# Kernel optimization log

Hardware: AMD Instinct MI355X
Metric: run time of the kernel (lower is better)

The kernel has to match this reference:

```python
import jax, jax.numpy as jnp
from jax import lax
import numpy as np

B, H, W, C = 32, 56, 56, 384
NH, WS, SS = 12, 7, 3
HD = C // NH
N = WS * WS
HID = 384  # int(mlp_ratio*dim / reduce_scale) = int(4*384/4)
SCALE = HD ** -0.5
L = H * W


def _rel_pos_index():
    coords = np.stack(np.meshgrid(np.arange(WS), np.arange(WS), indexing='ij'))
    cf = coords.reshape(2, -1)
    rc = (cf[:, :, None] - cf[:, None, :]).transpose(1, 2, 0)
    rc[..., 0] += WS - 1
    rc[..., 1] += WS - 1
    rc[..., 0] *= 2 * WS - 1
    return rc.sum(-1).reshape(-1)  # (N*N,)


def _win_part_np(x):
    b, h, w, c = x.shape
    x = x.reshape(b, h // WS, WS, w // WS, WS, c).transpose(0, 1, 3, 2, 4, 5)
    return x.reshape(-1, WS, WS, c)


def _attn_mask():
    img = np.zeros((1, H, W, 1), np.float32)
    cnt = 0
    sl = (slice(0, -WS), slice(-WS, -SS), slice(-SS, None))
    for hs in sl:
        for ws in sl:
            img[:, hs, ws, :] = cnt
            cnt += 1
    mw = _win_part_np(img).reshape(-1, N)
    am = mw[:, None, :] - mw[:, :, None]
    return np.where(am != 0, -100.0, 0.0).astype(np.float32)  # (nW, N, N)


REL_IDX = _rel_pos_index()
ATTN_MASK = _attn_mask()


def window_partition(x):  # (B,H,W,C) -> (B*nW, N, C)
    x = x.reshape(B, H // WS, WS, W // WS, WS, C).transpose(0, 1, 3, 2, 4, 5)
    return x.reshape(-1, N, C)


def window_reverse(wins):  # (B*nW, N, C) -> (B,H,W,C)
    x = wins.reshape(B, H // WS, W // WS, WS, WS, C).transpose(0, 1, 3, 2, 4, 5)
    return x.reshape(B, H, W, C)


def _ln(x, g, b):
    m = x.mean(-1, keepdims=True)
    v = ((x - m) ** 2).mean(-1, keepdims=True)
    return (x - m) * lax.rsqrt(v + 1e-5) * g + b


def setup_inputs() -> dict:
    key = jax.random.key(0)
    ks = iter(jax.random.split(key, 16))
    w = lambda shape: jax.random.normal(next(ks), shape, jnp.float32) * 0.02
    return {
        'x': jax.random.normal(next(ks), (B, L, C), jnp.float32),
        'norm1_g': jnp.ones((C,), jnp.float32), 'norm1_b': jnp.zeros((C,), jnp.float32),
        'qkv_w': w((3 * C, C)), 'qkv_b': jnp.zeros((3 * C,), jnp.float32),
        'rpb_table': w(((2 * WS - 1) ** 2, NH)),
        'proj_w': w((C, C)), 'proj_b': jnp.zeros((C,), jnp.float32),
        'se1_w': w((C // 2, C)), 'se1_b': jnp.zeros((C // 2,), jnp.float32),
        'se2_w': w((C, C // 2)), 'se2_b': jnp.zeros((C,), jnp.float32),
        'norm2_g': jnp.ones((C,), jnp.float32), 'norm2_b': jnp.zeros((C,), jnp.float32),
        'c1_w': w((HID, C)), 'c1_b': jnp.zeros((HID,), jnp.float32),
        'bn1_g': jnp.ones((HID,), jnp.float32), 'bn1_b': jnp.zeros((HID,), jnp.float32),
        'dw_w': w((HID, 1, 3, 3)), 'dw_b': jnp.zeros((HID,), jnp.float32),
        'bn2_g': jnp.ones((HID,), jnp.float32), 'bn2_b': jnp.zeros((HID,), jnp.float32),
        'c2_w': w((C, HID)), 'c2_b': jnp.zeros((C,), jnp.float32),
        'bn3_g': jnp.ones((C,), jnp.float32), 'bn3_b': jnp.zeros((C,), jnp.float32),
    }


def reference(x, norm1_g, norm1_b, qkv_w, qkv_b, rpb_table, proj_w, proj_b,
              se1_w, se1_b, se2_w, se2_b, norm2_g, norm2_b,
              c1_w, c1_b, bn1_g, bn1_b, dw_w, dw_b, bn2_g, bn2_b,
              c2_w, c2_b, bn3_g, bn3_b):
    shortcut = x
    h = _ln(x, norm1_g, norm1_b).reshape(B, H, W, C)
    h = jnp.roll(h, (-SS, -SS), axis=(1, 2))           # cyclic shift (SW-MSA)
    win = window_partition(h)                            # (B*nW, N, C)
    qkv = (win @ qkv_w.T + qkv_b).reshape(-1, N, 3, NH, HD).transpose(2, 0, 3, 1, 4)
    q, k, v = qkv[0] * SCALE, qkv[1], qkv[2]             # (B*nW, NH, N, HD)
    attn = jnp.einsum('bhnd,bhmd->bhnm', q, k)           # (B*nW, NH, N, N)
    rpb = rpb_table[jnp.asarray(REL_IDX)].reshape(N, N, NH).transpose(2, 0, 1)
    attn = attn + rpb[None]
    mask = jnp.asarray(ATTN_MASK)                        # (nW, N, N)
    nW = mask.shape[0]
    attn = (attn.reshape(B, nW, NH, N, N) + mask[None, :, None]).reshape(-1, NH, N, N)
    attn = jax.nn.softmax(attn, axis=-1)
    out = jnp.einsum('bhnm,bhmd->bhnd', attn, v).transpose(0, 2, 1, 3).reshape(-1, N, C)
    out = out @ proj_w.T + proj_b
    h = window_reverse(out)
    h = jnp.roll(h, (SS, SS), axis=(1, 2)).reshape(B, L, C)
    x = shortcut + h
    # SE gating, applied token-wise over channel dim exactly as ChannelSELayer_SA
    g = jax.nn.relu(x @ se1_w.T + se1_b)
    g = jax.nn.sigmoid(g @ se2_w.T + se2_b)
    x = x * g
    # light conv MLP branch (Mlp_Light); BatchNorm in eval mode with running
    # mean 0 / var 1 -> pure per-channel affine
    y = _ln(x, norm2_g, norm2_b).reshape(B, H, W, C).transpose(0, 3, 1, 2)  # NCHW
    y = jnp.einsum('bchw,oc->bohw', y, c1_w) + c1_b[None, :, None, None]     # 1x1 conv
    y = jax.nn.gelu(y, approximate=False) * bn1_g[None, :, None, None] + bn1_b[None, :, None, None]
    y = lax.conv_general_dilated(y, dw_w, (1, 1), 'SAME', feature_group_count=HID,
                                 dimension_numbers=('NCHW', 'OIHW', 'NCHW')) + dw_b[None, :, None, None]
    y = jax.nn.gelu(y, approximate=False) * bn2_g[None, :, None, None] + bn2_b[None, :, None, None]
    y = jnp.einsum('bchw,oc->bohw', y, c2_w) + c2_b[None, :, None, None]     # 1x1 conv
    y = y * bn3_g[None, :, None, None] + bn3_b[None, :, None, None]
    x = x + y.transpose(0, 2, 3, 1).reshape(B, L, C)
    return x
```

## Files before the change

kernel.cpp:

```cpp
#include <hip/hip_runtime.h>
#include <hip/hip_bf16.h>

typedef __attribute__((ext_vector_type(4))) float f32x4;
typedef __attribute__((ext_vector_type(8))) __bf16 bf16x8;
typedef __attribute__((ext_vector_type(8))) unsigned short u16x8;

#define SCALE_ 0.17677669529663687f
#define RS 19267584

#define OFF_R1 77070336ull
#define OFF_WB 154140672ull
#define OFF_WT 156205056ull
#define OFF_SB 156218880ull

__device__ __forceinline__ __bf16 tobf(float f) {
  __hip_bfloat16 h = __float2bfloat16(f);
  return __builtin_bit_cast(__bf16, h);
}
__device__ __forceinline__ unsigned short f2u(float f) {
  return __builtin_bit_cast(unsigned short, __float2bfloat16(f));
}

__global__ __launch_bounds__(256) void cvt_kernel(const float* __restrict__ src,
                                                  __hip_bfloat16* __restrict__ dst, int n) {
  int i = blockIdx.x * 256 + threadIdx.x;
  int stride = gridDim.x * 256;
  for (; i < n; i += stride) dst[i] = __float2bfloat16(src[i]);
}

__global__ __launch_bounds__(256) void dwrep_kernel(const float* __restrict__ src,
                                                    float* __restrict__ dst) {
  int i = blockIdx.x * 256 + threadIdx.x;
  if (i < 3456) {
    int c = i / 9, k = i - c * 9;
    dst[k * 384 + c] = src[i];
  }
}

__global__ __launch_bounds__(256) void c1prep_kernel(const float* __restrict__ c1w,
                                                     const float* __restrict__ c1b,
                                                     const float* __restrict__ g,
                                                     const float* __restrict__ b,
                                                     __hip_bfloat16* __restrict__ gc1,
                                                     float* __restrict__ S1,
                                                     float* __restrict__ bb) {
  const int n = blockIdx.x * 4 + (threadIdx.x >> 6);
  const int lane = threadIdx.x & 63;
  float s1 = 0.f, sb = 0.f;
  for (int k = lane; k < 384; k += 64) {
    float w = c1w[n * 384 + k];
    __hip_bfloat16 gw = __float2bfloat16(w * g[k]);
    gc1[n * 384 + k] = gw;
    s1 += __bfloat162float(gw);
    sb += w * b[k];
  }
#pragma unroll
  for (int m = 1; m < 64; m <<= 1) { s1 += __shfl_xor(s1, m, 64); sb += __shfl_xor(sb, m, 64); }
  if (lane == 0) { S1[n] = s1; bb[n] = c1b[n] + sb; }
}

template <bool WIN>
__global__ __launch_bounds__(256) void ln_kernel(const float* __restrict__ x,
                                                 const float* __restrict__ gm,
                                                 const float* __restrict__ bt,
                                                 __hip_bfloat16* __restrict__ out) {
  const int tok = blockIdx.x * 4 + (threadIdx.x >> 6);
  const int lane = threadIdx.x & 63;
  const float2* row = (const float2*)(x + (size_t)tok * 384);
  float2 v[3];
  v[0] = row[lane]; v[1] = row[lane + 64]; v[2] = row[lane + 128];
  float s = 0.f, sq = 0.f;
#pragma unroll
  for (int i = 0; i < 3; ++i) { s += v[i].x + v[i].y; sq += v[i].x * v[i].x + v[i].y * v[i].y; }
#pragma unroll
  for (int m = 1; m < 64; m <<= 1) { s += __shfl_xor(s, m, 64); sq += __shfl_xor(sq, m, 64); }
  const float mean = s * (1.f / 384.f);
  const float var = sq * (1.f / 384.f) - mean * mean;
  const float rstd = rsqrtf(var + 1e-5f);
  size_t dst;
  if constexpr (WIN) {
    int b = tok / 3136, l = tok - b * 3136;
    int i = l / 56, j = l - i * 56;
    int hp = i - 3; if (hp < 0) hp += 56;
    int wp = j - 3; if (wp < 0) wp += 56;
    int wi = (hp / 7) * 8 + wp / 7;
    int n = (hp % 7) * 7 + wp % 7;
    dst = (size_t)(b * 64 + wi) * 49 + n;
  } else {
    dst = (size_t)tok;
  }
  unsigned int* o = (unsigned int*)(out + dst * 384);
  const float2* G = (const float2*)gm;
  const float2* Bv = (const float2*)bt;
#pragma unroll
  for (int i = 0; i < 3; ++i) {
    int j = lane + 64 * i;
    float2 gv = G[j], bv = Bv[j];
    float a = (v[i].x - mean) * rstd * gv.x + bv.x;
    float b2 = (v[i].y - mean) * rstd * gv.y + bv.y;
    o[j] = (unsigned)f2u(a) | ((unsigned)f2u(b2) << 16);
  }
}

enum { EPI_SE2 = 2, EPI_C2 = 4, EPI_QKV = 5 };

template <int EPI, int KD>
__global__ __launch_bounds__(256) void gemm5(const __hip_bfloat16* __restrict__ Ap,
                                             const __hip_bfloat16* __restrict__ W,
                                             const float* __restrict__ bias,
                                             const float* __restrict__ p0,
                                             const float* __restrict__ p1,
                                             const float* __restrict__ p2,
                                             void* __restrict__ outp) {
  constexpr int KS = KD / 32;
  const int tid = threadIdx.x;
  const int lane = tid & 63, wave = tid >> 6;
  const int g = lane >> 4, r = lane & 15;
  const int row0 = blockIdx.x * 64;
  const int col0 = blockIdx.y * 192;
  const int n0 = wave * 48;

  __shared__ __align__(16) __hip_bfloat16 Al[64][40];
  __shared__ __align__(16) __hip_bfloat16 Bl[192][40];

  const int s_row = tid >> 2, s_c = (tid & 3) * 8;
  const size_t arow = (size_t)(row0 + s_row);

  f32x4 acc[4][3] = {};
  bf16x8 a_reg = *(const bf16x8*)(Ap + arow * KD + s_c);
  bf16x8 b_reg[3];
#pragma unroll
  for (int h = 0; h < 3; ++h)
    b_reg[h] = *(const bf16x8*)(W + (size_t)(col0 + s_row + 64 * h) * KD + s_c);

  for (int kk = 0; kk < KS; ++kk) {
    *(bf16x8*)(&Al[s_row][s_c]) = a_reg;
#pragma unroll
    for (int h = 0; h < 3; ++h) *(bf16x8*)(&Bl[s_row + 64 * h][s_c]) = b_reg[h];
    __syncthreads();
    if (kk + 1 < KS) {
      const int kb = (kk + 1) * 32 + s_c;
      a_reg = *(const bf16x8*)(Ap + arow * KD + kb);
#pragma unroll
      for (int h = 0; h < 3; ++h)
        b_reg[h] = *(const bf16x8*)(W + (size_t)(col0 + s_row + 64 * h) * KD + kb);
    }
    bf16x8 af[4];
#pragma unroll
    for (int mt = 0; mt < 4; ++mt) af[mt] = *(const bf16x8*)(&Al[mt * 16 + r][g * 8]);
#pragma unroll
    for (int nt = 0; nt < 3; ++nt) {
      bf16x8 bf = *(const bf16x8*)(&Bl[n0 + nt * 16 + r][g * 8]);
#pragma unroll
      for (int mt = 0; mt < 4; ++mt)
        acc[mt][nt] = __builtin_amdgcn_mfma_f32_16x16x32_bf16(af[mt], bf, acc[mt][nt], 0, 0, 0);
    }
    __syncthreads();
  }

#pragma unroll
  for (int mt = 0; mt < 4; ++mt) {
#pragma unroll
    for (int j = 0; j < 4; ++j) {
      const int row = row0 + mt * 16 + g * 4 + j;
#pragma unroll
      for (int nt = 0; nt < 3; ++nt) {
        const int col = col0 + n0 + nt * 16 + r;
        float v = acc[mt][nt][j] + bias[col];
        if constexpr (EPI == EPI_QKV) {
          const int s = col / 384, cs = col - s * 384;
          if (s == 0) v *= SCALE_;
          ((__hip_bfloat16*)outp)[(size_t)s * RS + (size_t)row * 384 + cs] = __float2bfloat16(v);
        } else if constexpr (EPI == EPI_SE2) {
          float gate = 1.f / (1.f + __expf(-v));
          ((float*)outp)[(size_t)row * 384 + col] = p0[(size_t)row * 384 + col] * gate;
        } else {
          float y = v * p0[col] + p1[col];
          ((float*)outp)[(size_t)row * 384 + col] = p2[(size_t)row * 384 + col] + y;
        }
      }
    }
  }
}

__global__ __launch_bounds__(256) void c1ln_kernel(const float* __restrict__ x2,
                                                   const __hip_bfloat16* __restrict__ gc1,
                                                   const float* __restrict__ S1,
                                                   const float* __restrict__ bb,
                                                   const float* __restrict__ bn1g_,
                                                   const float* __restrict__ bn1b_,
                                                   __hip_bfloat16* __restrict__ y1) {
  const int tid = threadIdx.x;
  const int lane = tid & 63, wave = tid >> 6;
  const int g = lane >> 4, r = lane & 15;
  const int row0 = blockIdx.x * 64;
  const int col0 = blockIdx.y * 192;
  const int n0 = wave * 48;

  __shared__ __align__(16) __hip_bfloat16 Al[64][40];
  __shared__ __align__(16) __hip_bfloat16 Bl[192][40];
  __shared__ float mean_l[64], rstd_l[64];

  const int s_row = tid >> 2, s_c = (tid & 3) * 8;
  const size_t abase = (size_t)(row0 + s_row) * 384;

  {
    float s = 0.f, sq = 0.f;
#pragma unroll
    for (int c = 0; c < 12; ++c) {
      const float4* p = (const float4*)(x2 + abase + c * 32 + s_c);
      float4 a = p[0], b = p[1];
      s += a.x + a.y + a.z + a.w + b.x + b.y + b.z + b.w;
      sq += a.x * a.x + a.y * a.y + a.z * a.z + a.w * a.w +
            b.x * b.x + b.y * b.y + b.z * b.z + b.w * b.w;
    }
#pragma unroll
    for (int m = 1; m < 4; m <<= 1) { s += __shfl_xor(s, m, 64); sq += __shfl_xor(sq, m, 64); }
    if ((tid & 3) == 0) {
      float mean = s * (1.f / 384.f);
      float var = sq * (1.f / 384.f) - mean * mean;
      mean_l[s_row] = mean;
      rstd_l[s_row] = rsqrtf(var + 1e-5f);
    }
  }
  __syncthreads();

  f32x4 acc[4][3] = {};
  bf16x8 a_reg;
  {
    const float4* sp = (const float4*)(x2 + abase + s_c);
    float4 a = sp[0], b = sp[1];
    a_reg[0] = tobf(a.x); a_reg[1] = tobf(a.y); a_reg[2] = tobf(a.z); a_reg[3] = tobf(a.w);
    a_reg[4] = tobf(b.x); a_reg[5] = tobf(b.y); a_reg[6] = tobf(b.z); a_reg[7] = tobf(b.w);
  }
  bf16x8 b_reg[3];
#pragma unroll
  for (int h = 0; h < 3; ++h)
    b_reg[h] = *(const bf16x8*)(gc1 + (size_t)(col0 + s_row + 64 * h) * 384 + s_c);

  for (int kk = 0; kk < 12; ++kk) {
    *(bf16x8*)(&Al[s_row][s_c]) = a_reg;
#pragma unroll
    for (int h = 0; h < 3; ++h) *(bf16x8*)(&Bl[s_row + 64 * h][s_c]) = b_reg[h];
    __syncthreads();
    if (kk + 1 < 12) {
      const int kb = (kk + 1) * 32 + s_c;
      const float4* sp = (const float4*)(x2 + abase + kb);
      float4 a = sp[0], b = sp[1];
      a_reg[0] = tobf(a.x); a_reg[1] = tobf(a.y); a_reg[2] = tobf(a.z); a_reg[3] = tobf(a.w);
      a_reg[4] = tobf(b.x); a_reg[5] = tobf(b.y); a_reg[6] = tobf(b.z); a_reg[7] = tobf(b.w);
#pragma unroll
      for (int h = 0; h < 3; ++h)
        b_reg[h] = *(const bf16x8*)(gc1 + (size_t)(col0 + s_row + 64 * h) * 384 + kb);
    }
    bf16x8 af[4];
#pragma unroll
    for (int mt = 0; mt < 4; ++mt) af[mt] = *(const bf16x8*)(&Al[mt * 16 + r][g * 8]);
#pragma unroll
    for (int nt = 0; nt < 3; ++nt) {
      bf16x8 bf = *(const bf16x8*)(&Bl[n0 + nt * 16 + r][g * 8]);
#pragma unroll
      for (int mt = 0; mt < 4; ++mt)
        acc[mt][nt] = __builtin_amdgcn_mfma_f32_16x16x32_bf16(af[mt], bf, acc[mt][nt], 0, 0, 0);
    }
    __syncthreads();
  }

#pragma unroll
  for (int mt = 0; mt < 4; ++mt) {
#pragma unroll
    for (int j = 0; j < 4; ++j) {
      const int rl = mt * 16 + g * 4 + j;
      const int row = row0 + rl;
      const float mean = mean_l[rl], rstd = rstd_l[rl];
#pragma unroll
      for (int nt = 0; nt < 3; ++nt) {
        const int col = col0 + n0 + nt * 16 + r;
        float v = rstd * (acc[mt][nt][j] - mean * S1[col]) + bb[col];
        float gl = 0.5f * v * (1.f + erff(v * 0.70710678118654752f));
        y1[(size_t)row * 384 + col] = __float2bfloat16(gl * bn1g_[col] + bn1b_[col]);
      }
    }
  }
}

__global__ __launch_bounds__(256) void gemm3_proj(const __hip_bfloat16* __restrict__ Ap,
                                                  const __hip_bfloat16* __restrict__ W,
                                                  const float* __restrict__ bias,
                                                  const float* __restrict__ p0,
                                                  void* __restrict__ outp,
                                                  const __hip_bfloat16* __restrict__ W2,
                                                  const float* __restrict__ bias2,
                                                  void* __restrict__ out2) {
  constexpr int NT = 6;
  const int tid = threadIdx.x;
  const int lane = tid & 63, wave = tid >> 6;
  const int g = lane >> 4, r = lane & 15;
  const int row0 = blockIdx.x * 64;
  const int n0 = wave * 96;

  __shared__ __align__(16) char smem[50176];
  auto Al = (__hip_bfloat16(*)[40])smem;
  auto Bl = (__hip_bfloat16(*)[40])(smem + 64 * 80);

  const int s_row = tid >> 2;
  const int s_c = (tid & 3) * 8;

  size_t arow;
  {
    int t = row0 + s_row;
    int b = t / 3136, l = t - b * 3136;
    int i = l / 56, j = l - i * 56;
    int hp = i >= 3 ? i - 3 : i + 53;
    int wp = j >= 3 ? j - 3 : j + 53;
    arow = ((size_t)(b * 64 + (hp / 7) * 8 + wp / 7)) * 49 + (hp % 7) * 7 + (wp % 7);
  }

  f32x4 acc[4][NT] = {};

  bf16x8 a_reg = *(const bf16x8*)(Ap + arow * 384 + s_c);
  bf16x8 b_reg[NT];
#pragma unroll
  for (int h = 0; h < NT; ++h)
    b_reg[h] = *(const bf16x8*)(W + (size_t)(s_row + 64 * h) * 384 + s_c);

  for (int kk = 0; kk < 12; ++kk) {
    *(bf16x8*)(&Al[s_row][s_c]) = a_reg;
#pragma unroll
    for (int h = 0; h < NT; ++h) *(bf16x8*)(&Bl[s_row + 64 * h][s_c]) = b_reg[h];
    __syncthreads();
    if (kk + 1 < 12) {
      const int kb = (kk + 1) * 32 + s_c;
      a_reg = *(const bf16x8*)(Ap + arow * 384 + kb);
#pragma unroll
      for (int h = 0; h < NT; ++h)
        b_reg[h] = *(const bf16x8*)(W + (size_t)(s_row + 64 * h) * 384 + kb);
    }
    bf16x8 af[4];
#pragma unroll
    for (int mt = 0; mt < 4; ++mt) af[mt] = *(const bf16x8*)(&Al[mt * 16 + r][g * 8]);
#pragma unroll
    for (int nt = 0; nt < NT; ++nt) {
      bf16x8 bf = *(const bf16x8*)(&Bl[n0 + nt * 16 + r][g * 8]);
#pragma unroll
      for (int mt = 0; mt < 4; ++mt)
        acc[mt][nt] = __builtin_amdgcn_mfma_f32_16x16x32_bf16(af[mt], bf, acc[mt][nt], 0, 0, 0);
    }
    __syncthreads();
  }

  auto Xt = (__hip_bfloat16(*)[392])smem;
#pragma unroll
  for (int mt = 0; mt < 4; ++mt)
#pragma unroll
    for (int j = 0; j < 4; ++j) {
      const int lrow = mt * 16 + g * 4 + j;
      const size_t ob = (size_t)(row0 + lrow) * 384;
#pragma unroll
      for (int nt = 0; nt < NT; ++nt) {
        const int col = n0 + nt * 16 + r;
        float v = acc[mt][nt][j] + bias[col] + p0[ob + col];
        ((float*)outp)[ob + col] = v;
        Xt[lrow][col] = __float2bfloat16(v);
      }
    }
  __syncthreads();
  f32x4 acc2[4][3] = {};
  const int c0 = wave * 48;
  for (int kk = 0; kk < 12; ++kk) {
    bf16x8 af2[4];
#pragma unroll
    for (int mt = 0; mt < 4; ++mt)
      af2[mt] = *(const bf16x8*)(&Xt[mt * 16 + r][kk * 32 + g * 8]);
#pragma unroll
    for (int nt2 = 0; nt2 < 3; ++nt2) {
      bf16x8 b2 = *(const bf16x8*)(W2 + (size_t)(c0 + nt2 * 16 + r) * 384 + kk * 32 + g * 8);
#pragma unroll
      for (int mt = 0; mt < 4; ++mt)
        acc2[mt][nt2] = __builtin_amdgcn_mfma_f32_16x16x32_bf16(af2[mt], b2, acc2[mt][nt2], 0, 0, 0);
    }
  }
#pragma unroll
  for (int mt = 0; mt < 4; ++mt)
#pragma unroll
    for (int j = 0; j < 4; ++j) {
      const size_t row = row0 + mt * 16 + g * 4 + j;
#pragma unroll
      for (int nt2 = 0; nt2 < 3; ++nt2) {
        const int col2 = c0 + nt2 * 16 + r;
        float v = acc2[mt][nt2][j] + bias2[col2];
        ((__hip_bfloat16*)out2)[row * 192 + col2] = __float2bfloat16(fmaxf(v, 0.f));
      }
    }
}

__global__ __launch_bounds__(64) void attn_core(const __hip_bfloat16* __restrict__ qkv,
                                                const float* __restrict__ rpb,
                                                __hip_bfloat16* __restrict__ ao, int win0) {
  const int bid = blockIdx.x;
  const int win_l = bid / 12, head = bid - win_l * 12;
  const int win = win0 + win_l;
  const int widx = win & 63;
  const int lane = threadIdx.x;
  const int g = lane >> 4, r = lane & 15;
  const int wbh = (widx >> 3) * 7, wbw = (widx & 7) * 7;
  const size_t rowbase = (size_t)(win_l * 49) * 384 + head * 32;
  const __hip_bfloat16* q_g = qkv + rowbase;
  const __hip_bfloat16* k_g = qkv + RS + rowbase;
  const __hip_bfloat16* v_g = qkv + 2 * RS + rowbase;

  __shared__ __align__(16) __hip_bfloat16 P_l[49 * 64];
  __shared__ __align__(16) unsigned short vT[32 * 72];

  bf16x8 zf;
#pragma unroll
  for (int i = 0; i < 8; ++i) zf[i] = tobf(0.f);

  for (int i = lane; i < 512; i += 64) {
    int d = i >> 4, t = 48 + (i & 15);
    vT[d * 72 + t] = 0;
  }
  if (lane < 49) {
#pragma unroll
    for (int c = 0; c < 4; ++c) {
      u16x8 vv = *(const u16x8*)(v_g + (size_t)lane * 384 + c * 8);
#pragma unroll
      for (int e = 0; e < 8; ++e) vT[(c * 8 + e) * 72 + lane] = vv[e];
    }
  }

  int yj4[4], xj4[4], rj4[4];
  bool val4[4];
#pragma unroll
  for (int nt = 0; nt < 4; ++nt) {
    int jt = nt * 16 + r;
    val4[nt] = jt < 49;
    int jc = val4[nt] ? jt : 0;
    int yj = jc / 7, xj = jc - yj * 7;
    yj4[nt] = yj; xj4[nt] = xj;
    int hj = wbh + yj, wj = wbw + xj;
    rj4[nt] = (hj < 49 ? 0 : (hj < 53 ? 1 : 2)) * 3 + (wj < 49 ? 0 : (wj < 53 ? 1 : 2));
  }

  f32x4 sA[4][4] = {};
  {
    bf16x8 qa[4];
#pragma unroll
    for (int mt = 0; mt < 4; ++mt) {
      int row = mt * 16 + r;
      qa[mt] = (row < 49) ? *(const bf16x8*)(q_g + (size_t)row * 384 + g * 8) : zf;
    }
#pragma unroll
    for (int nt = 0; nt < 4; ++nt) {
      int rowk = nt * 16 + r;
      bf16x8 kf = (rowk < 49) ? *(const bf16x8*)(k_g + (size_t)rowk * 384 + g * 8) : zf;
#pragma unroll
      for (int mt = 0; mt < 4; ++mt)
        sA[mt][nt] = __builtin_amdgcn_mfma_f32_16x16x32_bf16(qa[mt], kf, sA[mt][nt], 0, 0, 0);
    }
  }
#pragma unroll
  for (int mt = 0; mt < 4; ++mt) {
#pragma unroll
    for (int j = 0; j < 4; ++j) {
      const int it = mt * 16 + g * 4 + j;
      if (it < 49) {
        int yi = it / 7, xi = it - yi * 7;
        int hi = wbh + yi, wi2 = wbw + xi;
        int ri = (hi < 49 ? 0 : (hi < 53 ? 1 : 2)) * 3 + (wi2 < 49 ? 0 : (wi2 < 53 ? 1 : 2));
        float v4[4];
#pragma unroll
        for (int nt = 0; nt < 4; ++nt) {
          float sv = -1e30f;
          if (val4[nt]) {
            sv = sA[mt][nt][j] + rpb[((yi - yj4[nt] + 6) * 13 + (xi - xj4[nt] + 6)) * 12 + head];
            if (ri != rj4[nt]) sv -= 100.f;
          }
          v4[nt] = sv;
        }
        float mx = fmaxf(fmaxf(v4[0], v4[1]), fmaxf(v4[2], v4[3]));
#pragma unroll
        for (int m = 1; m < 16; m <<= 1) mx = fmaxf(mx, __shfl_xor(mx, m, 64));
        float sum = 0.f;
#pragma unroll
        for (int nt = 0; nt < 4; ++nt) { v4[nt] = __expf(v4[nt] - mx); sum += v4[nt]; }
#pragma unroll
        for (int m = 1; m < 16; m <<= 1) sum += __shfl_xor(sum, m, 64);
        float inv = 1.f / sum;
#pragma unroll
        for (int nt = 0; nt < 4; ++nt) {
          int col = nt * 16 + r;
          int swz = ((col >> 3) ^ (it & 7));
          P_l[it * 64 + swz * 8 + (col & 7)] = __float2bfloat16(v4[nt] * inv);
        }
      }
    }
  }
  f32x4 oA[4][2] = {};
#pragma unroll
  for (int ks = 0; ks < 2; ++ks) {
    bf16x8 pa[4];
#pragma unroll
    for (int mt = 0; mt < 4; ++mt) {
      int row = mt * 16 + r;
      int swz = (ks * 4 + g) ^ (row & 7);
      pa[mt] = (row < 49) ? *(const bf16x8*)(&P_l[row * 64 + swz * 8]) : zf;
    }
#pragma unroll
    for (int nt = 0; nt < 2; ++nt) {
      bf16x8 vbv = *(const bf16x8*)(&vT[(nt * 16 + r) * 72 + ks * 32 + g * 8]);
#pragma unroll
      for (int mt = 0; mt < 4; ++mt)
        oA[mt][nt] = __builtin_amdgcn_mfma_f32_16x16x32_bf16(pa[mt], vbv, oA[mt][nt], 0, 0, 0);
    }
  }
#pragma unroll
  for (int mt = 0; mt < 4; ++mt)
#pragma unroll
    for (int nt = 0; nt < 2; ++nt)
#pragma unroll
      for (int j = 0; j < 4; ++j) {
        int row = mt * 16 + g * 4 + j;
        if (row < 49)
          ao[((size_t)win * 49 + row) * 384 + head * 32 + nt * 16 + r] =
              __float2bfloat16(oA[mt][nt][j]);
      }
}

__global__ __launch_bounds__(256) void dw_kernel(const __hip_bfloat16* __restrict__ y1,
                                                 const float* __restrict__ wt,
                                                 const float* __restrict__ wb,
                                                 const float* __restrict__ g2,
                                                 const float* __restrict__ b2,
                                                 __hip_bfloat16* __restrict__ y2) {
  const int tid = blockIdx.x * 256 + threadIdx.x;
  const int c8 = tid % 48;
  int t = tid / 48;
  const int q = t & 3; t >>= 2;
  const int hq = t % 56;
  const int b = t / 56;
  const int cb = c8 * 8;
  const int x0 = q * 14;

  float wr[9][8];
#pragma unroll
  for (int k = 0; k < 9; ++k) {
    float4 a = *(const float4*)(wt + k * 384 + cb);
    float4 c = *(const float4*)(wt + k * 384 + cb + 4);
    wr[k][0] = a.x; wr[k][1] = a.y; wr[k][2] = a.z; wr[k][3] = a.w;
    wr[k][4] = c.x; wr[k][5] = c.y; wr[k][6] = c.z; wr[k][7] = c.w;
  }
  if (hq == 0) {
#pragma unroll
    for (int k = 0; k < 3; ++k)
#pragma unroll
      for (int i = 0; i < 8; ++i) wr[k][i] = 0.f;
  }
  if (hq == 55) {
#pragma unroll
    for (int k = 6; k < 9; ++k)
#pragma unroll
      for (int i = 0; i < 8; ++i) wr[k][i] = 0.f;
  }
  float bias[8], gv[8], bv[8];
  {
    float4 a = *(const float4*)(wb + cb), c = *(const float4*)(wb + cb + 4);
    bias[0] = a.x; bias[1] = a.y; bias[2] = a.z; bias[3] = a.w;
    bias[4] = c.x; bias[5] = c.y; bias[6] = c.z; bias[7] = c.w;
    float4 d = *(const float4*)(g2 + cb), e = *(const float4*)(g2 + cb + 4);
    gv[0] = d.x; gv[1] = d.y; gv[2] = d.z; gv[3] = d.w;
    gv[4] = e.x; gv[5] = e.y; gv[6] = e.z; gv[7] = e.w;
    float4 f = *(const float4*)(b2 + cb), h = *(const float4*)(b2 + cb + 4);
    bv[0] = f.x; bv[1] = f.y; bv[2] = f.z; bv[3] = f.w;
    bv[4] = h.x; bv[5] = h.y; bv[6] = h.z; bv[7] = h.w;
  }
  const int hm = hq > 0 ? hq - 1 : 0;
  const int hp = hq < 55 ? hq + 1 : 55;
  const __hip_bfloat16* r0 = y1 + ((size_t)(b * 3136 + hm * 56)) * 384 + cb;
  const __hip_bfloat16* r1 = y1 + ((size_t)(b * 3136 + hq * 56)) * 384 + cb;
  const __hip_bfloat16* r2 = y1 + ((size_t)(b * 3136 + hp * 56)) * 384 + cb;
  __hip_bfloat16* op = y2 + ((size_t)(b * 3136 + hq * 56)) * 384 + cb;

  u16x8 zv;
#pragma unroll
  for (int i = 0; i < 8; ++i) zv[i] = 0;
#define LDC(rp, x) (((unsigned)(x) < 56u) ? *(const u16x8*)((rp) + (size_t)(x) * 384) : zv)

  u16x8 L0 = LDC(r0, x0 - 1), L1 = LDC(r1, x0 - 1), L2 = LDC(r2, x0 - 1);
  u16x8 C0 = LDC(r0, x0), C1 = LDC(r1, x0), C2 = LDC(r2, x0);
#pragma unroll
  for (int xi = 0; xi < 14; ++xi) {
    const int x = x0 + xi;
    u16x8 R0 = LDC(r0, x + 1), R1 = LDC(r1, x + 1), R2 = LDC(r2, x + 1);
    float acc[8];
#pragma unroll
    for (int i = 0; i < 8; ++i) acc[i] = bias[i];
#pragma unroll
    for (int i = 0; i < 8; ++i) {
      acc[i] += __uint_as_float((unsigned)L0[i] << 16) * wr[0][i];
      acc[i] += __uint_as_float((unsigned)C0[i] << 16) * wr[1][i];
      acc[i] += __uint_as_float((unsigned)R0[i] << 16) * wr[2][i];
      acc[i] += __uint_as_float((unsigned)L1[i] << 16) * wr[3][i];
      acc[i] += __uint_as_float((unsigned)C1[i] << 16) * wr[4][i];
      acc[i] += __uint_as_float((unsigned)R1[i] << 16) * wr[5][i];
      acc[i] += __uint_as_float((unsigned)L2[i] << 16) * wr[6][i];
      acc[i] += __uint_as_float((unsigned)C2[i] << 16) * wr[7][i];
      acc[i] += __uint_as_float((unsigned)R2[i] << 16) * wr[8][i];
    }
    u16x8 o;
#pragma unroll
    for (int i = 0; i < 8; ++i) {
      float u = acc[i];
      float gl = 0.5f * u * (1.f + erff(u * 0.70710678118654752f));
      o[i] = f2u(gl * gv[i] + bv[i]);
    }
    *(u16x8*)(op + (size_t)x * 384) = o;
    L0 = C0; L1 = C1; L2 = C2;
    C0 = R0; C1 = R1; C2 = R2;
  }
#undef LDC
}

extern "C" void kernel_launch(void* const* d_in, const int* in_sizes, int n_in, void* d_out,
                              int out_size, void* d_ws, size_t ws_size, hipStream_t stream) {
  (void)in_sizes; (void)n_in; (void)out_size; (void)ws_size;
  const float* x = (const float*)d_in[0];
  const float* n1g = (const float*)d_in[1];
  const float* n1b = (const float*)d_in[2];
  const float* qkv_w = (const float*)d_in[3];
  const float* qkv_b = (const float*)d_in[4];
  const float* rpb = (const float*)d_in[5];
  const float* proj_w = (const float*)d_in[6];
  const float* proj_b = (const float*)d_in[7];
  const float* se1_w = (const float*)d_in[8];
  const float* se1_b = (const float*)d_in[9];
  const float* se2_w = (const float*)d_in[10];
  const float* se2_b = (const float*)d_in[11];
  const float* n2g = (const float*)d_in[12];
  const float* n2b = (const float*)d_in[13];
  const float* c1_w = (const float*)d_in[14];
  const float* c1_b = (const float*)d_in[15];
  const float* bn1g = (const float*)d_in[16];
  const float* bn1b = (const float*)d_in[17];
  const float* dw_w = (const float*)d_in[18];
  const float* dw_b = (const float*)d_in[19];
  const float* bn2g = (const float*)d_in[20];
  const float* bn2b = (const float*)d_in[21];
  const float* c2_w = (const float*)d_in[22];
  const float* c2_b = (const float*)d_in[23];
  const float* bn3g = (const float*)d_in[24];
  const float* bn3b = (const float*)d_in[25];

  char* ws = (char*)d_ws;
  __hip_bfloat16* r0b = (__hip_bfloat16*)ws;
  __hip_bfloat16* r1b = (__hip_bfloat16*)(ws + OFF_R1);
  __hip_bfloat16* wbp = (__hip_bfloat16*)(ws + OFF_WB);
  float* wt = (float*)(ws + OFF_WT);
  float* S1 = (float*)(ws + OFF_SB);
  float* bb = S1 + 384;
  __hip_bfloat16* qkv_wb = wbp;
  __hip_bfloat16* proj_wb = wbp + 442368;
  __hip_bfloat16* se1_wb = wbp + 589824;
  __hip_bfloat16* se2_wb = wbp + 663552;
  __hip_bfloat16* gc1 = wbp + 737280;
  __hip_bfloat16* c2_wb = wbp + 884736;
  float* out = (float*)d_out;

  cvt_kernel<<<1728, 256, 0, stream>>>(qkv_w, qkv_wb, 442368);
  cvt_kernel<<<576, 256, 0, stream>>>(proj_w, proj_wb, 147456);
  cvt_kernel<<<288, 256, 0, stream>>>(se1_w, se1_wb, 73728);
  cvt_kernel<<<288, 256, 0, stream>>>(se2_w, se2_wb, 73728);
  cvt_kernel<<<576, 256, 0, stream>>>(c2_w, c2_wb, 147456);
  c1prep_kernel<<<96, 256, 0, stream>>>(c1_w, c1_b, n2g, n2b, gc1, S1, bb);
  dwrep_kernel<<<14, 256, 0, stream>>>(dw_w, wt);

  ln_kernel<true><<<25088, 256, 0, stream>>>(x, n1g, n1b, r0b);

  for (int c = 0; c < 2; ++c) {
    const __hip_bfloat16* xa = r0b + (size_t)c * 50176 * 384;
    gemm5<EPI_QKV, 384><<<dim3(784, 6), 256, 0, stream>>>(
        xa, qkv_wb, qkv_b, nullptr, nullptr, nullptr, out);
    attn_core<<<12288, 64, 0, stream>>>((const __hip_bfloat16*)out, rpb, r0b, c * 1024);
  }

  gemm3_proj<<<1568, 256, 0, stream>>>(r0b, proj_wb, proj_b, x, out, se1_wb, se1_b, r1b);
  gemm5<EPI_SE2, 192><<<dim3(1568, 2), 256, 0, stream>>>(
      r1b, se2_wb, se2_b, out, nullptr, nullptr, out);
  c1ln_kernel<<<dim3(1568, 2), 256, 0, stream>>>(out, gc1, S1, bb, bn1g, bn1b, r1b);
  dw_kernel<<<1344, 256, 0, stream>>>(r1b, wt, dw_b, bn2g, bn2b, r0b);
  gemm5<EPI_C2, 384><<<dim3(1568, 2), 256, 0, stream>>>(
      r0b, c2_wb, c2_b, bn3g, bn3b, out, out);
}
```

Baseline: 924.5 us.

## Fuse LayerNorm statistics into SE gate GEMM and store residual in bf16

The SE second-layer GEMM becomes a dedicated kernel. Its epilogue applies the sigmoid gate and also computes per-row sum and sum-of-squares partials for the following LayerNorm. The c1ln kernel then reads these partials instead of re-reading the full fp32 activation to compute mean and variance. The projection kernel now stores the post-attention residual as bf16 rather than fp32, and the attention output halves are placed in spare buffer regions to make room, which cuts memory traffic at the cost of extra rounding in the residual path.

```diff
diff --git a/kernel.cpp b/kernel.cpp
--- a/kernel.cpp
+++ b/kernel.cpp
@@ -7,6 +7,7 @@
 
 #define SCALE_ 0.17677669529663687f
 #define RS 19267584
+#define HT 50176
 
 #define OFF_R1 77070336ull
 #define OFF_WB 154140672ull
@@ -102,7 +103,7 @@
   }
 }
 
-enum { EPI_SE2 = 2, EPI_C2 = 4, EPI_QKV = 5 };
+enum { EPI_C2 = 4, EPI_QKV = 5 };
 
 template <int EPI, int KD>
 __global__ __launch_bounds__(256) void gemm5(const __hip_bfloat16* __restrict__ Ap,
@@ -171,9 +172,6 @@
           const int s = col / 384, cs = col - s * 384;
           if (s == 0) v *= SCALE_;
           ((__hip_bfloat16*)outp)[(size_t)s * RS + (size_t)row * 384 + cs] = __float2bfloat16(v);
-        } else if constexpr (EPI == EPI_SE2) {
-          float gate = 1.f / (1.f + __expf(-v));
-          ((float*)outp)[(size_t)row * 384 + col] = p0[(size_t)row * 384 + col] * gate;
         } else {
           float y = v * p0[col] + p1[col];
           ((float*)outp)[(size_t)row * 384 + col] = p2[(size_t)row * 384 + col] + y;
@@ -183,7 +181,92 @@
   }
 }
 
+__global__ __launch_bounds__(256) void se2_kernel(const __hip_bfloat16* __restrict__ g1,
+                                                  const __hip_bfloat16* __restrict__ W,
+                                                  const float* __restrict__ bias,
+                                                  const __hip_bfloat16* __restrict__ x1b,
+                                                  float* __restrict__ x2out,
+                                                  float* __restrict__ stats) {
+  constexpr int KD = 192;
+  const int tid = threadIdx.x;
+  const int lane = tid & 63, wave = tid >> 6;
+  const int g = lane >> 4, r = lane & 15;
+  const int row0 = blockIdx.x * 64;
+  const int col0 = blockIdx.y * 192;
+  const int n0 = wave * 48;
+
+  __shared__ __align__(16) __hip_bfloat16 Al[64][40];
+  __shared__ __align__(16) __hip_bfloat16 Bl[192][40];
+  __shared__ float st[512];
+
+  const int s_row = tid >> 2, s_c = (tid & 3) * 8;
+  const size_t arow = (size_t)(row0 + s_row);
+
+  f32x4 acc[4][3] = {};
+  bf16x8 a_reg = *(const bf16x8*)(g1 + arow * KD + s_c);
+  bf16x8 b_reg[3];
+#pragma unroll
+  for (int h = 0; h < 3; ++h)
+    b_reg[h] = *(const bf16x8*)(W + (size_t)(col0 + s_row + 64 * h) * KD + s_c);
+
+  for (int kk = 0; kk < 6; ++kk) {
+    *(bf16x8*)(&Al[s_row][s_c]) = a_reg;
+#pragma unroll
+    for (int h = 0; h < 3; ++h) *(bf16x8*)(&Bl[s_row + 64 * h][s_c]) = b_reg[h];
+    __syncthreads();
+    if (kk + 1 < 6) {
+      const int kb = (kk + 1) * 32 + s_c;
+      a_reg = *(const bf16x8*)(g1 + arow * KD + kb);
+#pragma unroll
+      for (int h = 0; h < 3; ++h)
+        b_reg[h] = *(const bf16x8*)(W + (size_t)(col0 + s_row + 64 * h) * KD + kb);
+    }
+    bf16x8 af[4];
+#pragma unroll
+    for (int mt = 0; mt < 4; ++mt) af[mt] = *(const bf16x8*)(&Al[mt * 16 + r][g * 8]);
+#pragma unroll
+    for (int nt = 0; nt < 3; ++nt) {
+      bf16x8 bf = *(const bf16x8*)(&Bl[n0 + nt * 16 + r][g * 8]);
+#pragma unroll
+      for (int mt = 0; mt < 4; ++mt)
+        acc[mt][nt] = __builtin_amdgcn_mfma_f32_16x16x32_bf16(af[mt], bf, acc[mt][nt], 0, 0, 0);
+    }
+    __syncthreads();
+  }
+
+#pragma unroll
+  for (int mt = 0; mt < 4; ++mt) {
+#pragma unroll
+    for (int j = 0; j < 4; ++j) {
+      const int lrow = mt * 16 + g * 4 + j;
+      const size_t ob = (size_t)(row0 + lrow) * 384;
+      float s = 0.f, sq = 0.f;
+#pragma unroll
+      for (int nt = 0; nt < 3; ++nt) {
+        const int col = col0 + n0 + nt * 16 + r;
+        float v = acc[mt][nt][j] + bias[col];
+        float gate = 1.f / (1.f + __expf(-v));
+        float x1v = __bfloat162float(x1b[ob + col]);
+        float x2 = x1v * gate;
+        x2out[ob + col] = x2;
+        s += x2; sq += x2 * x2;
+      }
+#pragma unroll
+      for (int m = 1; m < 16; m <<= 1) { s += __shfl_xor(s, m, 64); sq += __shfl_xor(sq, m, 64); }
+      if (r == 0) { st[wave * 128 + lrow] = s; st[wave * 128 + 64 + lrow] = sq; }
+    }
+  }
+  __syncthreads();
+  if (tid < 64) {
+    float s = st[tid] + st[128 + tid] + st[256 + tid] + st[384 + tid];
+    float sq = st[64 + tid] + st[192 + tid] + st[320 + tid] + st[448 + tid];
+    stats[(size_t)(row0 + tid) * 4 + blockIdx.y * 2] = s;
+    stats[(size_t)(row0 + tid) * 4 + blockIdx.y * 2 + 1] = sq;
+  }
+}
+
 __global__ __launch_bounds__(256) void c1ln_kernel(const float* __restrict__ x2,
+                                                   const float* __restrict__ stats,
                                                    const __hip_bfloat16* __restrict__ gc1,
                                                    const float* __restrict__ S1,
                                                    const float* __restrict__ bb,
@@ -204,26 +287,15 @@
   const int s_row = tid >> 2, s_c = (tid & 3) * 8;
   const size_t abase = (size_t)(row0 + s_row) * 384;
 
-  {
-    float s = 0.f, sq = 0.f;
-#pragma unroll
-    for (int c = 0; c < 12; ++c) {
-      const float4* p = (const float4*)(x2 + abase + c * 32 + s_c);
-      float4 a = p[0], b = p[1];
-      s += a.x + a.y + a.z + a.w + b.x + b.y + b.z + b.w;
-      sq += a.x * a.x + a.y * a.y + a.z * a.z + a.w * a.w +
-            b.x * b.x + b.y * b.y + b.z * b.z + b.w * b.w;
-    }
-#pragma unroll
-    for (int m = 1; m < 4; m <<= 1) { s += __shfl_xor(s, m, 64); sq += __shfl_xor(sq, m, 64); }
-    if ((tid & 3) == 0) {
-      float mean = s * (1.f / 384.f);
-      float var = sq * (1.f / 384.f) - mean * mean;
-      mean_l[s_row] = mean;
-      rstd_l[s_row] = rsqrtf(var + 1e-5f);
-    }
-  }
-  __syncthreads();
+  if (tid < 64) {
+    const size_t row = row0 + tid;
+    float s = stats[row * 4] + stats[row * 4 + 2];
+    float sq = stats[row * 4 + 1] + stats[row * 4 + 3];
+    float mean = s * (1.f / 384.f);
+    float var = sq * (1.f / 384.f) - mean * mean;
+    mean_l[tid] = mean;
+    rstd_l[tid] = rsqrtf(var + 1e-5f);
+  }
 
   f32x4 acc[4][3] = {};
   bf16x8 a_reg;
@@ -284,14 +356,15 @@
   }
 }
 
-__global__ __launch_bounds__(256) void gemm3_proj(const __hip_bfloat16* __restrict__ Ap,
-                                                  const __hip_bfloat16* __restrict__ W,
-                                                  const float* __restrict__ bias,
-                                                  const float* __restrict__ p0,
-                                                  void* __restrict__ outp,
-                                                  const __hip_bfloat16* __restrict__ W2,
-                                                  const float* __restrict__ bias2,
-                                                  void* __restrict__ out2) {
+__global__ __launch_bounds__(256) void proj_kernel(const __hip_bfloat16* __restrict__ aoc0,
+                                                   const __hip_bfloat16* __restrict__ aoc1,
+                                                   const __hip_bfloat16* __restrict__ W,
+                                                   const float* __restrict__ bias,
+                                                   const float* __restrict__ x,
+                                                   __hip_bfloat16* __restrict__ x1b,
+                                                   const __hip_bfloat16* __restrict__ W2,
+                                                   const float* __restrict__ bias2,
+                                                   __hip_bfloat16* __restrict__ g1) {
   constexpr int NT = 6;
   const int tid = threadIdx.x;
   const int lane = tid & 63, wave = tid >> 6;
@@ -306,19 +379,20 @@
   const int s_row = tid >> 2;
   const int s_c = (tid & 3) * 8;
 
-  size_t arow;
+  const __hip_bfloat16* ap;
   {
     int t = row0 + s_row;
     int b = t / 3136, l = t - b * 3136;
     int i = l / 56, j = l - i * 56;
     int hp = i >= 3 ? i - 3 : i + 53;
     int wp = j >= 3 ? j - 3 : j + 53;
-    arow = ((size_t)(b * 64 + (hp / 7) * 8 + wp / 7)) * 49 + (hp % 7) * 7 + (wp % 7);
+    size_t arow = ((size_t)(b * 64 + (hp / 7) * 8 + wp / 7)) * 49 + (hp % 7) * 7 + (wp % 7);
+    ap = (arow < (size_t)HT) ? (aoc0 + arow * 384) : (aoc1 + (arow - HT) * 384);
   }
 
   f32x4 acc[4][NT] = {};
 
-  bf16x8 a_reg = *(const bf16x8*)(Ap + arow * 384 + s_c);
+  bf16x8 a_reg = *(const bf16x8*)(ap + s_c);
   bf16x8 b_reg[NT];
 #pragma unroll
   for (int h = 0; h < NT; ++h)
@@ -331,7 +405,7 @@
     __syncthreads();
     if (kk + 1 < 12) {
       const int kb = (kk + 1) * 32 + s_c;
-      a_reg = *(const bf16x8*)(Ap + arow * 384 + kb);
+      a_reg = *(const bf16x8*)(ap + kb);
 #pragma unroll
       for (int h = 0; h < NT; ++h)
         b_reg[h] = *(const bf16x8*)(W + (size_t)(s_row + 64 * h) * 384 + kb);
@@ -359,9 +433,10 @@
 #pragma unroll
       for (int nt = 0; nt < NT; ++nt) {
         const int col = n0 + nt * 16 + r;
-        float v = acc[mt][nt][j] + bias[col] + p0[ob + col];
-        ((float*)outp)[ob + col] = v;
-        Xt[lrow][col] = __float2bfloat16(v);
+        float v = acc[mt][nt][j] + bias[col] + x[ob + col];
+        __hip_bfloat16 hb = __float2bfloat16(v);
+        x1b[ob + col] = hb;
+        Xt[lrow][col] = hb;
       }
     }
   __syncthreads();
@@ -389,7 +464,7 @@
       for (int nt2 = 0; nt2 < 3; ++nt2) {
         const int col2 = c0 + nt2 * 16 + r;
         float v = acc2[mt][nt2][j] + bias2[col2];
-        ((__hip_bfloat16*)out2)[row * 192 + col2] = __float2bfloat16(fmaxf(v, 0.f));
+        g1[row * 192 + col2] = __float2bfloat16(fmaxf(v, 0.f));
       }
     }
 }
@@ -399,8 +474,7 @@
                                                 __hip_bfloat16* __restrict__ ao, int win0) {
   const int bid = blockIdx.x;
   const int win_l = bid / 12, head = bid - win_l * 12;
-  const int win = win0 + win_l;
-  const int widx = win & 63;
+  const int widx = (win0 + win_l) & 63;
   const int lane = threadIdx.x;
   const int g = lane >> 4, r = lane & 15;
   const int wbh = (widx >> 3) * 7, wbw = (widx & 7) * 7;
@@ -522,7 +596,7 @@
       for (int j = 0; j < 4; ++j) {
         int row = mt * 16 + g * 4 + j;
         if (row < 49)
-          ao[((size_t)win * 49 + row) * 384 + head * 32 + nt * 16 + r] =
+          ao[((size_t)win_l * 49 + row) * 384 + head * 32 + nt * 16 + r] =
               __float2bfloat16(oA[mt][nt][j]);
       }
 }
@@ -666,6 +740,11 @@
   __hip_bfloat16* c2_wb = wbp + 884736;
   float* out = (float*)d_out;
 
+  __hip_bfloat16* aoc0 = (__hip_bfloat16*)d_out + 3 * RS;
+  __hip_bfloat16* aoc1 = r0b;
+  __hip_bfloat16* g1 = r0b + (size_t)HT * 384;
+  float* stats = (float*)r0b;
+
   cvt_kernel<<<1728, 256, 0, stream>>>(qkv_w, qkv_wb, 442368);
   cvt_kernel<<<576, 256, 0, stream>>>(proj_w, proj_wb, 147456);
   cvt_kernel<<<288, 256, 0, stream>>>(se1_w, se1_wb, 73728);
@@ -677,16 +756,16 @@
   ln_kernel<true><<<25088, 256, 0, stream>>>(x, n1g, n1b, r0b);
 
   for (int c = 0; c < 2; ++c) {
-    const __hip_bfloat16* xa = r0b + (size_t)c * 50176 * 384;
+    const __hip_bfloat16* xa = r0b + (size_t)c * HT * 384;
     gemm5<EPI_QKV, 384><<<dim3(784, 6), 256, 0, stream>>>(
         xa, qkv_wb, qkv_b, nullptr, nullptr, nullptr, out);
-    attn_core<<<12288, 64, 0, stream>>>((const __hip_bfloat16*)out, rpb, r0b, c * 1024);
-  }
-
-  gemm3_proj<<<1568, 256, 0, stream>>>(r0b, proj_wb, proj_b, x, out, se1_wb, se1_b, r1b);
-  gemm5<EPI_SE2, 192><<<dim3(1568, 2), 256, 0, stream>>>(
-      r1b, se2_wb, se2_b, out, nullptr, nullptr, out);
-  c1ln_kernel<<<dim3(1568, 2), 256, 0, stream>>>(out, gc1, S1, bb, bn1g, bn1b, r1b);
+    attn_core<<<12288, 64, 0, stream>>>((const __hip_bfloat16*)out, rpb,
+                                        c == 0 ? aoc0 : aoc1, c * 1024);
+  }
+
+  proj_kernel<<<1568, 256, 0, stream>>>(aoc0, aoc1, proj_wb, proj_b, x, r1b, se1_wb, se1_b, g1);
+  se2_kernel<<<dim3(1568, 2), 256, 0, stream>>>(g1, se2_wb, se2_b, r1b, out, stats);
+  c1ln_kernel<<<dim3(1568, 2), 256, 0, stream>>>(out, stats, gc1, S1, bb, bn1g, bn1b, r1b);
   dw_kernel<<<1344, 256, 0, stream>>>(r1b, wt, dw_b, bn2g, bn2b, r0b);
   gemm5<EPI_C2, 384><<<dim3(1568, 2), 256, 0, stream>>>(
       r0b, c2_wb, c2_b, bn3g, bn3b, out, out);
```

New measurement: 901.0 us (median of 2 runs). 2.5% less time.
